# Optimization experiments

Hardware: AMD Instinct MI355X
Metric: run time of the kernel (lower is better)

Reference implementation:

```python
import jax, jax.numpy as jnp
import numpy as np
import math

B, S, D, H = 2, 2048, 1024, 16
DK = D // H
NUM_BUCKETS = 32
MAX_DISTANCE = 128


def _relative_position_bucket(relative_position, num_buckets=NUM_BUCKETS, max_distance=MAX_DISTANCE):
    # Bidirectional bucketing, faithful to the torch implementation.
    nb = num_buckets // 2
    n = -relative_position
    ret = (n < 0).astype(jnp.int32) * nb
    n = jnp.abs(n)
    max_exact = nb // 2
    is_small = n < max_exact
    # guard log(0); is_small branch covers n < max_exact anyway
    val_if_large = max_exact + (
        jnp.log(jnp.maximum(n, 1).astype(jnp.float32) / max_exact)
        / math.log(max_distance / max_exact)
        * (nb - max_exact)
    ).astype(jnp.int32)
    val_if_large = jnp.minimum(val_if_large, nb - 1)
    return ret + jnp.where(is_small, n, val_if_large)


def setup_inputs() -> dict:
    key = jax.random.key(0)
    ks = jax.random.split(key, 6)
    scale = 1.0 / math.sqrt(D)
    return {
        "hidden_states": jax.random.normal(ks[0], (B, S, D), dtype=jnp.float32),
        "Wq": jax.random.normal(ks[1], (D, D), dtype=jnp.float32) * scale,
        "Wk": jax.random.normal(ks[2], (D, D), dtype=jnp.float32) * scale,
        "Wv": jax.random.normal(ks[3], (D, D), dtype=jnp.float32) * scale,
        "Wo": jax.random.normal(ks[4], (D, D), dtype=jnp.float32) * scale,
        "rel_emb": jax.random.normal(ks[5], (NUM_BUCKETS, H), dtype=jnp.float32) * 0.1,
    }


def reference(hidden_states, Wq, Wk, Wv, Wo, rel_emb):
    b, s, d = hidden_states.shape
    # nn.Linear convention: y = x @ W.T
    q = jnp.einsum("bsd,ed->bse", hidden_states, Wq).reshape(b, s, H, DK).transpose(0, 2, 1, 3)
    k = jnp.einsum("bsd,ed->bse", hidden_states, Wk).reshape(b, s, H, DK).transpose(0, 2, 1, 3)
    v = jnp.einsum("bsd,ed->bse", hidden_states, Wv).reshape(b, s, H, DK).transpose(0, 2, 1, 3)
    scores = jnp.einsum("bhqd,bhkd->bhqk", q, k) / math.sqrt(DK)  # [B,H,S,S]
    # T5 relative position bias
    ctx = jnp.arange(s)[:, None]
    mem = jnp.arange(s)[None, :]
    rp_bucket = _relative_position_bucket(mem - ctx)          # [S,S]
    bias = rel_emb[rp_bucket]                                  # [S,S,H]
    bias = bias.transpose(2, 0, 1)[None]                       # [1,H,S,S]
    scores = scores + bias
    attn = jax.nn.softmax(scores, axis=-1)
    out = jnp.einsum("bhqk,bhkd->bhqd", attn, v)               # [B,H,S,DK]
    out = out.transpose(0, 2, 1, 3).reshape(b, s, d)
    return jnp.einsum("bsd,ed->bse", out, Wo)
```

## Files before the change

### kernel.cpp

```cpp
#include <hip/hip_runtime.h>
#include <hip/hip_bf16.h>
#include <cstdint>
#include <cstddef>

typedef __bf16 bf16;
typedef __attribute__((ext_vector_type(8))) __bf16 bf16x8;
typedef __attribute__((ext_vector_type(4))) __bf16 bf16x4;
typedef __attribute__((ext_vector_type(4))) float f32x4;
typedef __attribute__((ext_vector_type(4))) short s16x4;

#define B_ 2
#define S_ 2048
#define D_ 1024
#define H_ 16
#define DK_ 64
#define NROWS (B_*S_)
#define NBIAS 4095
#define LDQ 3072
#define LOG2E 1.44269504f

__device__ __forceinline__ void async16(void* lds, const void* g) {
  __builtin_amdgcn_global_load_lds(
      (const __attribute__((address_space(1))) void*)g,
      (__attribute__((address_space(3))) void*)lds, 16, 0, 0);
}

__device__ __forceinline__ f32x4 mfma16(bf16x8 a, bf16x8 b, f32x4 c) {
  return __builtin_amdgcn_mfma_f32_16x16x32_bf16(a, b, c, 0, 0, 0);
}

__device__ __forceinline__ s16x4 bc4(bf16x4 x) {
  union { bf16x4 b; s16x4 s; } u; u.b = x; return u.s;
}

__device__ __forceinline__ f32x4 mfma16k(bf16x4 a, bf16x4 b, f32x4 c) {
  return __builtin_amdgcn_mfma_f32_16x16x16bf16_1k(bc4(a), bc4(b), c, 0, 0, 0);
}

__device__ __forceinline__ float exp2_hw(float x) {
  return __builtin_amdgcn_exp2f(x);
}

__global__ void cvt_kernel(const float* __restrict__ in, bf16* __restrict__ out, int n4) {
  int i = blockIdx.x * blockDim.x + threadIdx.x;
  if (i >= n4) return;
  float4 v = ((const float4*)in)[i];
  bf16x4 o;
  o[0] = (bf16)v.x; o[1] = (bf16)v.y; o[2] = (bf16)v.z; o[3] = (bf16)v.w;
  ((bf16x4*)out)[i] = o;
}

__global__ void cvt_w_kernel(const float* __restrict__ a, const float* __restrict__ b,
                             const float* __restrict__ c, const float* __restrict__ d,
                             bf16* __restrict__ oqkv, bf16* __restrict__ oo) {
  const int y = blockIdx.y;
  const float* src = (y == 0) ? a : (y == 1) ? b : (y == 2) ? c : d;
  bf16* dst = (y < 3) ? (oqkv + (size_t)y * D_ * D_) : oo;
  int i = blockIdx.x * 256 + threadIdx.x;
  float4 v = ((const float4*)src)[i];
  bf16x4 o;
  o[0] = (bf16)v.x; o[1] = (bf16)v.y; o[2] = (bf16)v.z; o[3] = (bf16)v.w;
  ((bf16x4*)dst)[i] = o;
}

__global__ void bias_kernel(const float* __restrict__ rel_emb, float* __restrict__ tab) {
  int idx = blockIdx.x * 256 + threadIdx.x;
  if (idx >= H_ * NBIAS) return;
  int h = idx / NBIAS;
  int p = idx - h * NBIAS;
  int rel = p - 2047;
  int n = -rel;
  int ret = 0;
  if (n < 0) { ret = 16; n = -n; }
  int bucket;
  if (n < 8) {
    bucket = ret + n;
  } else {
    double v = log((double)n / 8.0) / log(16.0) * 8.0;
    int vi = 8 + (int)v;
    if (vi > 15) vi = 15;
    bucket = ret + vi;
  }
  tab[idx] = rel_emb[bucket * H_ + h] * LOG2E;
}

template<int OUT_BF16, int MF>
__global__ __launch_bounds__(256, 3)
void gemm_bt(const bf16* __restrict__ A, const bf16* __restrict__ Bw,
             void* __restrict__ C, int M, int N, int K,
             int colThr, float a0, float a1) {
  __shared__ bf16 As[MF * 32 * 64];
  __shared__ bf16 Bs[128 * 64];
  const int tid = threadIdx.x;
  const int lane = tid & 63;
  const int w = tid >> 6;
  const int wr = w >> 1, wc = w & 1;
  const int l15 = lane & 15, lhi = lane >> 4;
  const int m0 = blockIdx.y * (MF * 32), n0 = blockIdx.x * 128;
  const float alpha = (n0 < colThr) ? a0 : a1;

  f32x4 acc[MF][4] = {};

  const int urow = tid >> 3;
  const int uswz = (tid & 7) ^ (urow & 7);
  const bf16* ga = A  + (size_t)(m0 + urow) * K + uswz * 8;
  const bf16* gb = Bw + (size_t)(n0 + urow) * K + uswz * 8;

  for (int kt = 0; kt < K; kt += 64) {
#pragma unroll
    for (int rnd = 0; rnd < MF; ++rnd)
      async16(As + tid * 8 + rnd * 2048, ga + kt + (size_t)(rnd * 32) * K);
#pragma unroll
    for (int rnd = 0; rnd < 4; ++rnd)
      async16(Bs + tid * 8 + rnd * 2048, gb + kt + (size_t)(rnd * 32) * K);
    __syncthreads();

#pragma unroll
    for (int kc = 0; kc < 2; ++kc) {
      bf16x8 af[MF], bfr[4];
#pragma unroll
      for (int m = 0; m < MF; ++m) {
        int row = wr * (MF * 16) + m * 16 + l15;
        int off = (row * 64 + kc * 32 + lhi * 8) ^ ((row & 7) << 3);
        af[m] = *(const bf16x8*)&As[off];
      }
#pragma unroll
      for (int n = 0; n < 4; ++n) {
        int row = wc * 64 + n * 16 + l15;
        int off = (row * 64 + kc * 32 + lhi * 8) ^ ((row & 7) << 3);
        bfr[n] = *(const bf16x8*)&Bs[off];
      }
      __builtin_amdgcn_s_setprio(1);
#pragma unroll
      for (int m = 0; m < MF; ++m)
#pragma unroll
        for (int n = 0; n < 4; ++n)
          acc[m][n] = mfma16(af[m], bfr[n], acc[m][n]);
      __builtin_amdgcn_s_setprio(0);
    }
    __syncthreads();
  }

#pragma unroll
  for (int m = 0; m < MF; ++m)
#pragma unroll
    for (int n = 0; n < 4; ++n)
#pragma unroll
      for (int r = 0; r < 4; ++r) {
        int row = m0 + wr * (MF * 16) + m * 16 + lhi * 4 + r;
        int col = n0 + wc * 64 + n * 16 + l15;
        float v = acc[m][n][r] * alpha;
        if (OUT_BF16) ((bf16*)C)[(size_t)row * N + col] = (bf16)v;
        else          ((float*)C)[(size_t)row * N + col] = v;
      }
}

__global__ __launch_bounds__(256)
void transpose_v(const bf16* __restrict__ Q, bf16* __restrict__ VT) {
  const int t = threadIdx.x;
  const int ms = t >> 4, md = t & 15;
  const int s0 = blockIdx.x * 128, d0 = blockIdx.y * 128, b = blockIdx.z;
  bf16x8 in[8];
  const bf16* src = Q + (size_t)(b * 2048 + s0 + ms * 8) * LDQ + 2048 + d0 + md * 8;
#pragma unroll
  for (int i = 0; i < 8; ++i) in[i] = *(const bf16x8*)(src + (size_t)i * LDQ);
  bf16* dst = VT + (size_t)(b * 1024 + d0 + md * 8) * 2048 + s0 + ms * 8;
#pragma unroll
  for (int j = 0; j < 8; ++j) {
    bf16x8 o;
#pragma unroll
    for (int i = 0; i < 8; ++i) o[i] = in[i][j];
    *(bf16x8*)(dst + (size_t)j * 2048) = o;
  }
}

__global__ __launch_bounds__(256, 4)
void attn_fwd(const bf16* __restrict__ QKV, const bf16* __restrict__ VTg_,
              const float* __restrict__ biasTab, const float* __restrict__ rel_emb,
              bf16* __restrict__ Og) {
  __shared__ bf16 Ks[2][64 * 64];
  __shared__ bf16 VTs[2][64 * 64];
  __shared__ float bias_s[512];
  const int tid = threadIdx.x;
  const int lane = tid & 63, w = tid >> 6;
  const int l15 = lane & 15, lhi = lane >> 4;
  const int wg = blockIdx.x;
  const int bh = wg & 31, qt = wg >> 5;
  const int b = bh >> 4, h = bh & 15;
  const int q0 = qt * 64;

  for (int i = tid; i < 512; i += 256)
    bias_s[i] = biasTab[h * NBIAS + 1791 + i];

  const float cL = rel_emb[15 * H_ + h] * LOG2E;
  const float cR = rel_emb[31 * H_ + h] * LOG2E;

  bf16x8 qa[2];
  {
    const bf16* Qbase = QKV + (size_t)(b * S_ + q0 + w * 16) * LDQ + h * DK_;
#pragma unroll
    for (int c = 0; c < 2; ++c)
      qa[c] = *(const bf16x8*)(Qbase + (size_t)l15 * LDQ + c * 32 + lhi * 8);
  }

  int koff[8];
#pragma unroll
  for (int kf = 0; kf < 4; ++kf)
#pragma unroll
    for (int c = 0; c < 2; ++c) {
      int krow = kf * 16 + l15;
      koff[kf * 2 + c] = ((krow * 64 + c * 32 + lhi * 8) ^ ((krow & 7) << 3)) * 2;
    }
  int voff[16];
#pragma unroll
  for (int df = 0; df < 4; ++df)
#pragma unroll
    for (int kf = 0; kf < 4; ++kf)
      voff[df * 4 + kf] =
          (((df * 16 + l15) * 64 + kf * 16 + lhi * 4) * 2) ^ ((l15 & 7) << 4);

  float lpart = 0.f;
  f32x4 oacc[4] = {};

  const int urow = tid >> 3;
  const int uswz = (tid & 7) ^ (urow & 7);
  const bf16* gk = QKV  + (size_t)(b * S_) * LDQ + 1024 + h * DK_
                        + (size_t)urow * LDQ + uswz * 8;
  const bf16* gv = VTg_ + (size_t)(b * 1024 + h * DK_) * 2048
                        + (size_t)urow * 2048 + uswz * 8;

  async16(&Ks[0][tid * 8],         gk);
  async16(&Ks[0][tid * 8 + 2048],  gk + 32 * LDQ);
  async16(&VTs[0][tid * 8],        gv);
  async16(&VTs[0][tid * 8 + 2048], gv + 32 * 2048);
  gk += 64 * LDQ;
  gv += 64;
  __syncthreads();

#define TILE_BODY(CUR, KT, DO_PF)                                              \
  do {                                                                         \
    if (DO_PF) {                                                               \
      async16(&Ks[(CUR) ^ 1][tid * 8],         gk);                            \
      async16(&Ks[(CUR) ^ 1][tid * 8 + 2048],  gk + 32 * LDQ);                 \
      async16(&VTs[(CUR) ^ 1][tid * 8],        gv);                            \
      async16(&VTs[(CUR) ^ 1][tid * 8 + 2048], gv + 32 * 2048);                \
      gk += 64 * LDQ;                                                          \
      gv += 64;                                                                \
    }                                                                          \
    const int dk0 = (KT) - q0;                                                 \
    f32x4 st[4];                                                               \
    if (dk0 >= -128 && dk0 <= 128) {                                           \
      const int bb0 = dk0 + lhi * 4 - (w * 16 + l15) + 256;                    \
      _Pragma("unroll")                                                        \
      for (int kf = 0; kf < 4; ++kf)                                           \
        _Pragma("unroll")                                                      \
        for (int r = 0; r < 4; ++r)                                            \
          st[kf][r] = bias_s[bb0 + kf * 16 + r];                               \
    } else {                                                                   \
      const float cq = (dk0 > 0) ? cR : cL;                                    \
      _Pragma("unroll")                                                        \
      for (int kf = 0; kf < 4; ++kf)                                           \
        _Pragma("unroll")                                                      \
        for (int r = 0; r < 4; ++r)                                            \
          st[kf][r] = cq;                                                      \
    }                                                                          \
    _Pragma("unroll")                                                          \
    for (int kf = 0; kf < 4; ++kf) {                                           \
      _Pragma("unroll")                                                        \
      for (int c = 0; c < 2; ++c) {                                            \
        bf16x8 kb = *(const bf16x8*)((const char*)&Ks[CUR][0] +                \
                                     koff[kf * 2 + c]);                        \
        st[kf] = mfma16(kb, qa[c], st[kf]);                                    \
      }                                                                        \
    }                                                                          \
    bf16x4 pa[4];                                                              \
    float rs = 0.f;                                                            \
    _Pragma("unroll")                                                          \
    for (int kf = 0; kf < 4; ++kf)                                             \
      _Pragma("unroll")                                                        \
      for (int r = 0; r < 4; ++r) {                                            \
        float p = exp2_hw(st[kf][r]);                                          \
        rs += p;                                                               \
        pa[kf][r] = (bf16)p;                                                   \
      }                                                                        \
    lpart += rs;                                                               \
    _Pragma("unroll")                                                          \
    for (int df = 0; df < 4; ++df) {                                           \
      bf16x4 vb[4];                                                            \
      _Pragma("unroll")                                                        \
      for (int kf = 0; kf < 4; ++kf)                                           \
        vb[kf] = *(const bf16x4*)((const char*)&VTs[CUR][0] +                  \
                                  voff[df * 4 + kf]);                          \
      _Pragma("unroll")                                                        \
      for (int kf = 0; kf < 4; ++kf)                                           \
        oacc[df] = mfma16k(pa[kf], vb[kf], oacc[df]);                          \
    }                                                                          \
    __syncthreads();                                                           \
  } while (0)

  for (int tt = 0; tt < 16; ++tt) {
    const int ktbase = tt * 128;
    TILE_BODY(0, ktbase, true);
    TILE_BODY(1, ktbase + 64, tt < 15);
  }
#undef TILE_BODY

  float lr0 = lpart;
  lr0 += __shfl_xor(lr0, 16);
  lr0 += __shfl_xor(lr0, 32);
#pragma unroll
  for (int r = 0; r < 4; ++r) {
    float lr = __shfl(lr0, lhi * 4 + r);
    float inv = 1.0f / lr;
#pragma unroll
    for (int df = 0; df < 4; ++df) {
      int row = b * S_ + q0 + w * 16 + lhi * 4 + r;
      int col = h * DK_ + df * 16 + l15;
      Og[(size_t)row * D_ + col] = (bf16)(oacc[df][r] * inv);
    }
  }
}

extern "C" void kernel_launch(void* const* d_in, const int* in_sizes, int n_in,
                              void* d_out, int out_size, void* d_ws, size_t ws_size,
                              hipStream_t stream) {
  const float* X   = (const float*)d_in[0];
  const float* Wq  = (const float*)d_in[1];
  const float* Wk  = (const float*)d_in[2];
  const float* Wv  = (const float*)d_in[3];
  const float* Wo  = (const float*)d_in[4];
  const float* rel = (const float*)d_in[5];
  float* out = (float*)d_out;
  char* ws = (char*)d_ws;
  const size_t MB = 1u << 20;
  bf16* Xb    = (bf16*)(ws + 0 * MB);
  bf16* Wqkvb = (bf16*)(ws + 8 * MB);
  bf16* Wob   = (bf16*)(ws + 14 * MB);
  bf16* QKVb  = (bf16*)(ws + 16 * MB);
  bf16* VTb   = (bf16*)(ws + 40 * MB);
  float* biasTab = (float*)(ws + 48 * MB);

  cvt_kernel<<<4096, 256, 0, stream>>>(X, Xb, NROWS * D_ / 4);
  cvt_w_kernel<<<dim3(1024, 4), 256, 0, stream>>>(Wq, Wk, Wv, Wo, Wqkvb, Wob);
  bias_kernel<<<256, 256, 0, stream>>>(rel, biasTab);

  gemm_bt<1, 4><<<dim3(24, 32), 256, 0, stream>>>(Xb, Wqkvb, QKVb,
      NROWS, 3 * D_, D_, 1024, 0.125f * LOG2E, 1.0f);

  transpose_v<<<dim3(16, 8, 2), 256, 0, stream>>>(QKVb, VTb);

  attn_fwd<<<1024, 256, 0, stream>>>(QKVb, VTb, biasTab, rel, Xb );

  gemm_bt<0, 2><<<dim3(8, 64), 256, 0, stream>>>(Xb, Wob, out,
      NROWS, D_, D_, 0, 1.0f, 1.0f);
}
```

Before: 120.7 us.

## Fuse prep conversions into one kernel and write V transposed from QKV GEMM epilogue

Merges the three preprocessing kernels (X conversion, weight conversion, bias table) into one launch, branching on block index. Removes the separate transpose_v kernel: QKV GEMM blocks covering the V columns stage their tile in shared memory with a swizzle and write V transposed directly to VT. This cuts two launches and one read and write pass over V, in exchange for a more complex epilogue and V no longer being written to the QKV buffer.

Result: faster. 114.9 us, median of 2 (-4.8%).

```diff
diff --git a/kernel.cpp b/kernel.cpp
--- a/kernel.cpp
+++ b/kernel.cpp
@@ -41,56 +41,60 @@
   return __builtin_amdgcn_exp2f(x);
 }
 
-__global__ void cvt_kernel(const float* __restrict__ in, bf16* __restrict__ out, int n4) {
-  int i = blockIdx.x * blockDim.x + threadIdx.x;
-  if (i >= n4) return;
-  float4 v = ((const float4*)in)[i];
-  bf16x4 o;
-  o[0] = (bf16)v.x; o[1] = (bf16)v.y; o[2] = (bf16)v.z; o[3] = (bf16)v.w;
-  ((bf16x4*)out)[i] = o;
-}
-
-__global__ void cvt_w_kernel(const float* __restrict__ a, const float* __restrict__ b,
-                             const float* __restrict__ c, const float* __restrict__ d,
-                             bf16* __restrict__ oqkv, bf16* __restrict__ oo) {
-  const int y = blockIdx.y;
-  const float* src = (y == 0) ? a : (y == 1) ? b : (y == 2) ? c : d;
-  bf16* dst = (y < 3) ? (oqkv + (size_t)y * D_ * D_) : oo;
-  int i = blockIdx.x * 256 + threadIdx.x;
-  float4 v = ((const float4*)src)[i];
-  bf16x4 o;
-  o[0] = (bf16)v.x; o[1] = (bf16)v.y; o[2] = (bf16)v.z; o[3] = (bf16)v.w;
-  ((bf16x4*)dst)[i] = o;
-}
-
-__global__ void bias_kernel(const float* __restrict__ rel_emb, float* __restrict__ tab) {
-  int idx = blockIdx.x * 256 + threadIdx.x;
-  if (idx >= H_ * NBIAS) return;
-  int h = idx / NBIAS;
-  int p = idx - h * NBIAS;
-  int rel = p - 2047;
-  int n = -rel;
-  int ret = 0;
-  if (n < 0) { ret = 16; n = -n; }
-  int bucket;
-  if (n < 8) {
-    bucket = ret + n;
+__global__ void prep_kernel(const float* __restrict__ X,
+                            const float* __restrict__ Wq, const float* __restrict__ Wk,
+                            const float* __restrict__ Wv, const float* __restrict__ Wo,
+                            const float* __restrict__ rel_emb,
+                            bf16* __restrict__ Xb, bf16* __restrict__ oqkv,
+                            bf16* __restrict__ oo, float* __restrict__ tab) {
+  const int bid = blockIdx.x;
+  const int tid = threadIdx.x;
+  if (bid < 4096) {
+    int i = bid * 256 + tid;
+    float4 v = ((const float4*)X)[i];
+    bf16x4 o;
+    o[0] = (bf16)v.x; o[1] = (bf16)v.y; o[2] = (bf16)v.z; o[3] = (bf16)v.w;
+    ((bf16x4*)Xb)[i] = o;
+  } else if (bid < 8192) {
+    int widx = bid - 4096;
+    int y = widx >> 10;
+    const float* src = (y == 0) ? Wq : (y == 1) ? Wk : (y == 2) ? Wv : Wo;
+    bf16* dst = (y < 3) ? (oqkv + (size_t)y * D_ * D_) : oo;
+    int i = (widx & 1023) * 256 + tid;
+    float4 v = ((const float4*)src)[i];
+    bf16x4 o;
+    o[0] = (bf16)v.x; o[1] = (bf16)v.y; o[2] = (bf16)v.z; o[3] = (bf16)v.w;
+    ((bf16x4*)dst)[i] = o;
   } else {
-    double v = log((double)n / 8.0) / log(16.0) * 8.0;
-    int vi = 8 + (int)v;
-    if (vi > 15) vi = 15;
-    bucket = ret + vi;
-  }
-  tab[idx] = rel_emb[bucket * H_ + h] * LOG2E;
-}
-
-template<int OUT_BF16, int MF>
+    int idx = (bid - 8192) * 256 + tid;
+    if (idx >= H_ * NBIAS) return;
+    int h = idx / NBIAS;
+    int p = idx - h * NBIAS;
+    int rel = p - 2047;
+    int n = -rel;
+    int ret = 0;
+    if (n < 0) { ret = 16; n = -n; }
+    int bucket;
+    if (n < 8) {
+      bucket = ret + n;
+    } else {
+      double v = log((double)n / 8.0) / log(16.0) * 8.0;
+      int vi = 8 + (int)v;
+      if (vi > 15) vi = 15;
+      bucket = ret + vi;
+    }
+    tab[idx] = rel_emb[bucket * H_ + h] * LOG2E;
+  }
+}
+
+template<int OUT_BF16, int MF, int VT_EP>
 __global__ __launch_bounds__(256, 3)
 void gemm_bt(const bf16* __restrict__ A, const bf16* __restrict__ Bw,
-             void* __restrict__ C, int M, int N, int K,
-             int colThr, float a0, float a1) {
-  __shared__ bf16 As[MF * 32 * 64];
-  __shared__ bf16 Bs[128 * 64];
+             void* __restrict__ C, bf16* __restrict__ VT, int vThr,
+             int M, int N, int K, int colThr, float a0, float a1) {
+  __shared__ bf16 smem[MF * 32 * 64 + 128 * 64];
+  bf16* As = smem;
+  bf16* Bs = smem + MF * 32 * 64;
   const int tid = threadIdx.x;
   const int lane = tid & 63;
   const int w = tid >> 6;
@@ -141,6 +145,31 @@
     __syncthreads();
   }
 
+  if (VT_EP && n0 >= vThr) {
+    bf16* T = smem;
+#pragma unroll
+    for (int m = 0; m < MF; ++m)
+#pragma unroll
+      for (int n = 0; n < 4; ++n)
+#pragma unroll
+        for (int r = 0; r < 4; ++r) {
+          int rl = wr * (MF * 16) + m * 16 + lhi * 4 + r;
+          int cl = wc * 64 + n * 16 + l15;
+          T[cl * 128 + (rl ^ ((cl & 7) << 3))] = (bf16)(acc[m][n][r] * alpha);
+        }
+    __syncthreads();
+    const int bb = m0 >> 11, s0l = m0 & 2047, d0 = n0 - vThr;
+    const int dr = tid >> 1, sh = tid & 1;
+    bf16* dst = VT + ((size_t)(bb * 1024 + d0 + dr)) * 2048 + s0l + sh * 64;
+    const bf16* src = T + dr * 128;
+#pragma unroll
+    for (int i = 0; i < 8; ++i) {
+      int sb = sh * 8 + i;
+      *(bf16x8*)(dst + i * 8) = *(const bf16x8*)(src + ((sb ^ (dr & 7)) * 8));
+    }
+    return;
+  }
+
 #pragma unroll
   for (int m = 0; m < MF; ++m)
 #pragma unroll
@@ -153,25 +182,6 @@
         if (OUT_BF16) ((bf16*)C)[(size_t)row * N + col] = (bf16)v;
         else          ((float*)C)[(size_t)row * N + col] = v;
       }
-}
-
-__global__ __launch_bounds__(256)
-void transpose_v(const bf16* __restrict__ Q, bf16* __restrict__ VT) {
-  const int t = threadIdx.x;
-  const int ms = t >> 4, md = t & 15;
-  const int s0 = blockIdx.x * 128, d0 = blockIdx.y * 128, b = blockIdx.z;
-  bf16x8 in[8];
-  const bf16* src = Q + (size_t)(b * 2048 + s0 + ms * 8) * LDQ + 2048 + d0 + md * 8;
-#pragma unroll
-  for (int i = 0; i < 8; ++i) in[i] = *(const bf16x8*)(src + (size_t)i * LDQ);
-  bf16* dst = VT + (size_t)(b * 1024 + d0 + md * 8) * 2048 + s0 + ms * 8;
-#pragma unroll
-  for (int j = 0; j < 8; ++j) {
-    bf16x8 o;
-#pragma unroll
-    for (int i = 0; i < 8; ++i) o[i] = in[i][j];
-    *(bf16x8*)(dst + (size_t)j * 2048) = o;
-  }
 }
 
 __global__ __launch_bounds__(256, 4)
@@ -340,17 +350,16 @@
   bf16* VTb   = (bf16*)(ws + 40 * MB);
   float* biasTab = (float*)(ws + 48 * MB);
 
-  cvt_kernel<<<4096, 256, 0, stream>>>(X, Xb, NROWS * D_ / 4);
-  cvt_w_kernel<<<dim3(1024, 4), 256, 0, stream>>>(Wq, Wk, Wv, Wo, Wqkvb, Wob);
-  bias_kernel<<<256, 256, 0, stream>>>(rel, biasTab);
-
-  gemm_bt<1, 4><<<dim3(24, 32), 256, 0, stream>>>(Xb, Wqkvb, QKVb,
+  prep_kernel<<<8448, 256, 0, stream>>>(X, Wq, Wk, Wv, Wo, rel,
+                                        Xb, Wqkvb, Wob, biasTab);
+
+  gemm_bt<1, 4, 1><<<dim3(24, 32), 256, 0, stream>>>(Xb, Wqkvb, QKVb,
+      VTb, 2048,
       NROWS, 3 * D_, D_, 1024, 0.125f * LOG2E, 1.0f);
 
-  transpose_v<<<dim3(16, 8, 2), 256, 0, stream>>>(QKVb, VTb);
-
   attn_fwd<<<1024, 256, 0, stream>>>(QKVb, VTb, biasTab, rel, Xb );
 
-  gemm_bt<0, 2><<<dim3(8, 64), 256, 0, stream>>>(Xb, Wob, out,
+  gemm_bt<0, 2, 0><<<dim3(8, 64), 256, 0, stream>>>(Xb, Wob, out,
+      nullptr, 1 << 30,
       NROWS, D_, D_, 0, 1.0f, 1.0f);
 }
```
